# Kernel optimization log

Measured on AMD Instinct MI355X. Metric: run time of the kernel, lower is better.

Reference implementation:

```python
import jax, jax.numpy as jnp
import numpy as np

U, I, D = 100000, 150000, 64
N = U + I
E = 1250000
KEEP_RATE = 0.8


def setup_inputs() -> dict:
    key = jax.random.key(0)
    k1, k2, k3, k4, k5, k6 = jax.random.split(key, 6)
    row = jax.random.randint(k1, (E,), 0, N, dtype=jnp.int32)
    col = jax.random.randint(k2, (E,), 0, N, dtype=jnp.int32)
    adj_values = jax.random.uniform(k3, (E,), dtype=jnp.float32)
    # edge dropout mask: floor(rand + keep_rate) in {0,1}, exactly as SpAdjEdgeDrop
    edge_mask = jnp.floor(jax.random.uniform(k4, (E,), dtype=jnp.float32) + KEEP_RATE)
    user_embeds = jax.random.normal(k5, (U, D), dtype=jnp.float32)
    item_embeds = jax.random.normal(k6, (I, D), dtype=jnp.float32)
    return {
        "row": row,
        "col": col,
        "adj_values": adj_values,
        "edge_mask": edge_mask,
        "user_embeds": user_embeds,
        "item_embeds": item_embeds,
        "layer_num": 3,
    }


def reference(row, col, adj_values, edge_mask, user_embeds, item_embeds, layer_num):
    user_num = user_embeds.shape[0]
    n_nodes = user_num + item_embeds.shape[0]
    # edge-dropped sparse values (mask==0 edges contribute nothing to spmm)
    vals = adj_values * edge_mask  # [E]
    embeds = jnp.concatenate([user_embeds, item_embeds], axis=0)  # [N, D]
    acc = embeds
    cur = embeds
    for _ in range(layer_num):
        # spmm: out[r] += vals[e] * cur[c] for each edge e=(r,c)
        msgs = vals[:, None] * cur[col]  # [E, D] gather
        cur = jax.ops.segment_sum(msgs, row, num_segments=n_nodes)  # [N, D] scatter-add
        acc = acc + cur
    out = acc / (layer_num + 1)
    return out[:user_num], out[user_num:]
```

## Files before the change

kernel.cpp:

```cpp
#include <hip/hip_runtime.h>


#define U_NODES 100000
#define N_NODES 250000
#define DIM4 16
#define E_EDGES 1250000
#define TILE_ROWS 1024
#define NT 245
#define CAP 6144
#define P1_BLOCKS 512

typedef unsigned short u16;

__device__ __forceinline__ float bf2f(u16 h) {
    return __uint_as_float(((unsigned)h) << 16);
}
__device__ __forceinline__ u16 f2bf(float f) {
    unsigned u = __float_as_uint(f);
    u += 0x7fffu + ((u >> 16) & 1u);
    return (u16)(u >> 16);
}
__device__ __forceinline__ ushort4 gat(const u16* __restrict__ base, int node, int part) {
    return ((const ushort4*)(base + ((size_t)node << 6)))[part];
}
__device__ __forceinline__ void fma4(float4& s, float v, ushort4 h) {
    s.x += v * bf2f(h.x);
    s.y += v * bf2f(h.y);
    s.z += v * bf2f(h.z);
    s.w += v * bf2f(h.w);
}

__global__ void lgcn_part(const float4* __restrict__ user4,
                          const float4* __restrict__ item4,
                          u16* __restrict__ e0b,
                          const int* __restrict__ row,
                          const int* __restrict__ col,
                          const float* __restrict__ adj,
                          const float* __restrict__ mask,
                          int* __restrict__ cursors,
                          int2* __restrict__ staging) {
    __shared__ int lhist[NT];
    __shared__ int lbase[NT];
    const int t = threadIdx.x;
    const int gsz = gridDim.x * blockDim.x;
    const int g0 = blockIdx.x * blockDim.x + t;

    for (int i = t; i < NT; i += 256) lhist[i] = 0;
    __syncthreads();

    for (int e = g0; e < E_EDGES; e += gsz)
        if (mask[e] != 0.0f) atomicAdd(&lhist[row[e] >> 10], 1);
    __syncthreads();

    for (int i = t; i < NT; i += 256) {
        int c = lhist[i];
        lbase[i] = c ? atomicAdd(&cursors[i * 16], c) : 0;
        lhist[i] = 0;
    }

    const int CONV = N_NODES * 8;
    for (int i = g0; i < CONV; i += gsz) {
        const int uc = U_NODES * 8;
        const float4* src = (i < uc) ? (user4 + 2 * (long)i)
                                     : (item4 + 2 * (long)(i - uc));
        float4 a = src[0];
        float4 b = src[1];
        int4 o;
        o.x = (int)((unsigned)f2bf(a.x) | ((unsigned)f2bf(a.y) << 16));
        o.y = (int)((unsigned)f2bf(a.z) | ((unsigned)f2bf(a.w) << 16));
        o.z = (int)((unsigned)f2bf(b.x) | ((unsigned)f2bf(b.y) << 16));
        o.w = (int)((unsigned)f2bf(b.z) | ((unsigned)f2bf(b.w) << 16));
        ((int4*)e0b)[i] = o;
    }
    __syncthreads();

    for (int e = g0; e < E_EDGES; e += gsz) {
        float m = mask[e];
        if (m == 0.0f) continue;
        int r = row[e];
        int bkt = r >> 10;
        int rank = lbase[bkt] + atomicAdd(&lhist[bkt], 1);
        if (rank < CAP)
            staging[(size_t)bkt * CAP + rank] =
                make_int2(((r & 1023) << 18) | col[e], __float_as_int(adj[e] * m));
    }
}

__global__ void lgcn_build(const int* __restrict__ cursors,
                           const int2* __restrict__ staging,
                           int* __restrict__ total,
                           int2* __restrict__ rowdesc,
                           int2* __restrict__ csr) {
    __shared__ int lcount[TILE_ROWS];
    __shared__ int lstart[TILE_ROWS];
    __shared__ int lcur[TILE_ROWS];
    __shared__ int lscan[256];
    __shared__ int sbase;
    const int b = blockIdx.x;
    const int t = threadIdx.x;
    const int2* sp = staging + (size_t)b * CAP;
    int cnt = cursors[b * 16];
    if (cnt > CAP) cnt = CAP;

    lcount[t] = 0; lcount[t + 256] = 0; lcount[t + 512] = 0; lcount[t + 768] = 0;
    __syncthreads();
    for (int i = t; i < cnt; i += 256)
        atomicAdd(&lcount[((unsigned)sp[i].x) >> 18], 1);
    __syncthreads();

    int c0 = lcount[4 * t + 0], c1 = lcount[4 * t + 1];
    int c2 = lcount[4 * t + 2], c3 = lcount[4 * t + 3];
    int p0 = (c0 + 3) & ~3, p1 = (c1 + 3) & ~3, p2 = (c2 + 3) & ~3, p3 = (c3 + 3) & ~3;
    int s = p0 + p1 + p2 + p3;
    lscan[t] = s;
    __syncthreads();
    for (int off = 1; off < 256; off <<= 1) {
        int v = (t >= off) ? lscan[t - off] : 0;
        __syncthreads();
        if (t >= off) lscan[t] += v;
        __syncthreads();
    }
    if (t == 255) sbase = atomicAdd(total, lscan[255]);
    __syncthreads();
    const int tilesum = lscan[255];
    int pos = sbase + lscan[t] - s;
    int rbase = b * TILE_ROWS + 4 * t;
    if (rbase + 0 < N_NODES) rowdesc[rbase + 0] = make_int2(pos, c0);
    lstart[4 * t + 0] = pos; lcur[4 * t + 0] = 0; pos += p0;
    if (rbase + 1 < N_NODES) rowdesc[rbase + 1] = make_int2(pos, c1);
    lstart[4 * t + 1] = pos; lcur[4 * t + 1] = 0; pos += p1;
    if (rbase + 2 < N_NODES) rowdesc[rbase + 2] = make_int2(pos, c2);
    lstart[4 * t + 2] = pos; lcur[4 * t + 2] = 0; pos += p2;
    if (rbase + 3 < N_NODES) rowdesc[rbase + 3] = make_int2(pos, c3);
    lstart[4 * t + 3] = pos; lcur[4 * t + 3] = 0;
    __syncthreads();

    for (int i = t; i < tilesum; i += 256) csr[sbase + i] = make_int2(0, 0);
    __syncthreads();

    for (int i = t; i < cnt; i += 256) {
        int2 rec = sp[i];
        int rw = ((unsigned)rec.x) >> 18;
        int rank = atomicAdd(&lcur[rw], 1);
        csr[lstart[rw] + rank] = make_int2(rec.x & 0x3FFFF, rec.y);
    }
}

template <bool LAST>
__global__ void lgcn_pull(const int2* __restrict__ rowdesc,
                          const int2* __restrict__ csr,
                          const u16*  __restrict__ curb,
                          const u16*  __restrict__ e0b,
                          const u16*  __restrict__ e1b,
                          u16*        __restrict__ outb,
                          float4*     __restrict__ out) {
    int tid = blockIdx.x * blockDim.x + threadIdx.x;
    int r = tid >> 4;
    int part = tid & 15;
    if (r >= N_NODES) return;
    int2 rd = rowdesc[r];
    int start = rd.x;
    int pend  = start + ((rd.y + 3) & ~3);
    float4 s = make_float4(0.f, 0.f, 0.f, 0.f);
    int e = start;
    for (; e + 8 <= pend; e += 8) {
        int4 ca = *(const int4*)(csr + e);
        int4 cb = *(const int4*)(csr + e + 2);
        int4 cc = *(const int4*)(csr + e + 4);
        int4 cd = *(const int4*)(csr + e + 6);
        ushort4 h0 = gat(curb, ca.x, part);
        ushort4 h1 = gat(curb, ca.z, part);
        ushort4 h2 = gat(curb, cb.x, part);
        ushort4 h3 = gat(curb, cb.z, part);
        ushort4 h4 = gat(curb, cc.x, part);
        ushort4 h5 = gat(curb, cc.z, part);
        ushort4 h6 = gat(curb, cd.x, part);
        ushort4 h7 = gat(curb, cd.z, part);
        fma4(s, __int_as_float(ca.y), h0);
        fma4(s, __int_as_float(ca.w), h1);
        fma4(s, __int_as_float(cb.y), h2);
        fma4(s, __int_as_float(cb.w), h3);
        fma4(s, __int_as_float(cc.y), h4);
        fma4(s, __int_as_float(cc.w), h5);
        fma4(s, __int_as_float(cd.y), h6);
        fma4(s, __int_as_float(cd.w), h7);
    }
    if (e < pend) {
        int4 ca = *(const int4*)(csr + e);
        int4 cb = *(const int4*)(csr + e + 2);
        ushort4 h0 = gat(curb, ca.x, part);
        ushort4 h1 = gat(curb, ca.z, part);
        ushort4 h2 = gat(curb, cb.x, part);
        ushort4 h3 = gat(curb, cb.z, part);
        fma4(s, __int_as_float(ca.y), h0);
        fma4(s, __int_as_float(ca.w), h1);
        fma4(s, __int_as_float(cb.y), h2);
        fma4(s, __int_as_float(cb.w), h3);
    }
    size_t oi = (size_t)r * DIM4 + part;
    if (LAST) {
        ushort4 a0 = ((const ushort4*)e0b)[oi];
        ushort4 a1 = ((const ushort4*)e1b)[oi];
        ushort4 a2 = ((const ushort4*)curb)[oi];
        out[oi] = make_float4(
            (s.x + bf2f(a0.x) + bf2f(a1.x) + bf2f(a2.x)) * 0.25f,
            (s.y + bf2f(a0.y) + bf2f(a1.y) + bf2f(a2.y)) * 0.25f,
            (s.z + bf2f(a0.z) + bf2f(a1.z) + bf2f(a2.z)) * 0.25f,
            (s.w + bf2f(a0.w) + bf2f(a1.w) + bf2f(a2.w)) * 0.25f);
    } else {
        ((ushort4*)outb)[oi] = make_ushort4(f2bf(s.x), f2bf(s.y), f2bf(s.z), f2bf(s.w));
    }
}

extern "C" void kernel_launch(void* const* d_in, const int* in_sizes, int n_in,
                              void* d_out, int out_size, void* d_ws, size_t ws_size,
                              hipStream_t stream) {
    const int*   row  = (const int*)d_in[0];
    const int*   col  = (const int*)d_in[1];
    const float* adj  = (const float*)d_in[2];
    const float* mask = (const float*)d_in[3];
    const float4* user4 = (const float4*)d_in[4];
    const float4* item4 = (const float4*)d_in[5];

    float4* acc = (float4*)d_out;

    const size_t bemb_bytes = (size_t)N_NODES * 64 * sizeof(u16);
    char* p = (char*)d_ws;
    u16* e0b = (u16*)p;  p += bemb_bytes;
    u16* e1b = (u16*)p;  p += bemb_bytes;
    u16* e2b = (u16*)p;  p += bemb_bytes;
    int* total   = (int*)p;
    int* cursors = (int*)(p + 64);
    p += 64 + (size_t)NT * 64;
    int2* staging = (int2*)p;  p += (size_t)NT * CAP * 8;
    int2* rowdesc = (int2*)p;  p += ((size_t)N_NODES * 8 + 63) & ~63ul;
    int2* csr     = (int2*)p;

    const int BLK = 256;
    const long node_vec4 = (long)N_NODES * DIM4;
    const int  grid_pull = (int)((node_vec4 + BLK - 1) / BLK);

    hipMemsetAsync(total, 0, 64 + (size_t)NT * 64, stream);
    lgcn_part<<<P1_BLOCKS, BLK, 0, stream>>>(user4, item4, e0b, row, col, adj, mask,
                                             cursors, staging);
    lgcn_build<<<NT, BLK, 0, stream>>>(cursors, staging, total, rowdesc, csr);

    lgcn_pull<false><<<grid_pull, BLK, 0, stream>>>(rowdesc, csr, e0b, nullptr, nullptr, e1b, nullptr);
    lgcn_pull<false><<<grid_pull, BLK, 0, stream>>>(rowdesc, csr, e1b, nullptr, nullptr, e2b, nullptr);
    lgcn_pull<true ><<<grid_pull, BLK, 0, stream>>>(rowdesc, csr, e2b, e0b, e1b, nullptr, acc);
}
```

Measured before the change: 296.9 us.

## Replace global bucket cursors with per-block staging segments and offset table

The partition kernel now writes each block's kept edges into its own fixed-size staging segment, ordered by bucket using a local prefix scan. It records per-block bucket offsets in a table, replacing global atomic cursors and the capped shared buckets. The build kernel rebuilds each bucket's edge list by scanning those per-block counts and binary-searching the source segment for every element. This removes global atomics and the CAP overflow limit. In exchange it adds two binary searches per edge and scattered reads across 1024 segments.

```diff
diff --git a/kernel.cpp b/kernel.cpp
--- a/kernel.cpp
+++ b/kernel.cpp
@@ -7,8 +7,9 @@
 #define E_EDGES 1250000
 #define TILE_ROWS 1024
 #define NT 245
-#define CAP 6144
-#define P1_BLOCKS 512
+#define NB 1024
+#define GSZ (NB * 256)
+#define BSEG 1280
 
 typedef unsigned short u16;
 
@@ -37,109 +38,147 @@
                           const int* __restrict__ col,
                           const float* __restrict__ adj,
                           const float* __restrict__ mask,
-                          int* __restrict__ cursors,
+                          int* __restrict__ OFF,
                           int2* __restrict__ staging) {
-    __shared__ int lhist[NT];
-    __shared__ int lbase[NT];
+    __shared__ int lhist[256];
+    __shared__ int lscan[256];
+    __shared__ int loff[256];
+    __shared__ int lcur[256];
     const int t = threadIdx.x;
-    const int gsz = gridDim.x * blockDim.x;
-    const int g0 = blockIdx.x * blockDim.x + t;
-
-    for (int i = t; i < NT; i += 256) lhist[i] = 0;
-    __syncthreads();
-
-    for (int e = g0; e < E_EDGES; e += gsz)
+    const int b = blockIdx.x;
+    const int g0 = b * 256 + t;
+
+    lhist[t] = 0;
+    __syncthreads();
+
+    for (int e = g0; e < E_EDGES; e += GSZ)
         if (mask[e] != 0.0f) atomicAdd(&lhist[row[e] >> 10], 1);
     __syncthreads();
 
-    for (int i = t; i < NT; i += 256) {
-        int c = lhist[i];
-        lbase[i] = c ? atomicAdd(&cursors[i * 16], c) : 0;
-        lhist[i] = 0;
+    int v = lhist[t];
+    lscan[t] = v;
+    __syncthreads();
+    for (int off = 1; off < 256; off <<= 1) {
+        int u = (t >= off) ? lscan[t - off] : 0;
+        __syncthreads();
+        if (t >= off) lscan[t] += u;
+        __syncthreads();
+    }
+    loff[t] = lscan[t] - v;
+    lcur[t] = 0;
+    __syncthreads();
+
+    OFF[b * 256 + t] = loff[t];
+
+    for (int e = g0; e < E_EDGES; e += GSZ) {
+        float m = mask[e];
+        if (m == 0.0f) continue;
+        int r = row[e];
+        int bkt = r >> 10;
+        int rank = loff[bkt] + atomicAdd(&lcur[bkt], 1);
+        staging[(size_t)b * BSEG + rank] =
+            make_int2(((r & 1023) << 18) | col[e], __float_as_int(adj[e] * m));
     }
 
     const int CONV = N_NODES * 8;
-    for (int i = g0; i < CONV; i += gsz) {
+    for (int i = g0; i < CONV; i += GSZ) {
         const int uc = U_NODES * 8;
         const float4* src = (i < uc) ? (user4 + 2 * (long)i)
                                      : (item4 + 2 * (long)(i - uc));
         float4 a = src[0];
-        float4 b = src[1];
+        float4 bb = src[1];
         int4 o;
         o.x = (int)((unsigned)f2bf(a.x) | ((unsigned)f2bf(a.y) << 16));
         o.y = (int)((unsigned)f2bf(a.z) | ((unsigned)f2bf(a.w) << 16));
-        o.z = (int)((unsigned)f2bf(b.x) | ((unsigned)f2bf(b.y) << 16));
-        o.w = (int)((unsigned)f2bf(b.z) | ((unsigned)f2bf(b.w) << 16));
+        o.z = (int)((unsigned)f2bf(bb.x) | ((unsigned)f2bf(bb.y) << 16));
+        o.w = (int)((unsigned)f2bf(bb.z) | ((unsigned)f2bf(bb.w) << 16));
         ((int4*)e0b)[i] = o;
     }
-    __syncthreads();
-
-    for (int e = g0; e < E_EDGES; e += gsz) {
-        float m = mask[e];
-        if (m == 0.0f) continue;
-        int r = row[e];
-        int bkt = r >> 10;
-        int rank = lbase[bkt] + atomicAdd(&lhist[bkt], 1);
-        if (rank < CAP)
-            staging[(size_t)bkt * CAP + rank] =
-                make_int2(((r & 1023) << 18) | col[e], __float_as_int(adj[e] * m));
-    }
-}
-
-__global__ void lgcn_build(const int* __restrict__ cursors,
+}
+
+__global__ void lgcn_build(const int* __restrict__ OFF,
                            const int2* __restrict__ staging,
                            int* __restrict__ total,
                            int2* __restrict__ rowdesc,
                            int2* __restrict__ csr) {
+    __shared__ int S[NB];
+    __shared__ int boff[NB];
     __shared__ int lcount[TILE_ROWS];
     __shared__ int lstart[TILE_ROWS];
     __shared__ int lcur[TILE_ROWS];
     __shared__ int lscan[256];
     __shared__ int sbase;
-    const int b = blockIdx.x;
+    const int i = blockIdx.x;
     const int t = threadIdx.x;
-    const int2* sp = staging + (size_t)b * CAP;
-    int cnt = cursors[b * 16];
-    if (cnt > CAP) cnt = CAP;
-
+
+    int o0 = OFF[(4 * t + 0) * 256 + i], e0 = OFF[(4 * t + 0) * 256 + i + 1];
+    int o1 = OFF[(4 * t + 1) * 256 + i], e1 = OFF[(4 * t + 1) * 256 + i + 1];
+    int o2 = OFF[(4 * t + 2) * 256 + i], e2 = OFF[(4 * t + 2) * 256 + i + 1];
+    int o3 = OFF[(4 * t + 3) * 256 + i], e3 = OFF[(4 * t + 3) * 256 + i + 1];
+    int c0 = e0 - o0, c1 = e1 - o1, c2 = e2 - o2, c3 = e3 - o3;
+    boff[4 * t + 0] = o0; boff[4 * t + 1] = o1;
+    boff[4 * t + 2] = o2; boff[4 * t + 3] = o3;
+    int sl = c0 + c1 + c2 + c3;
+    lscan[t] = sl;
+    __syncthreads();
+    for (int off = 1; off < 256; off <<= 1) {
+        int u = (t >= off) ? lscan[t - off] : 0;
+        __syncthreads();
+        if (t >= off) lscan[t] += u;
+        __syncthreads();
+    }
+    int ex = lscan[t] - sl;
+    S[4 * t + 0] = ex;
+    S[4 * t + 1] = ex + c0;
+    S[4 * t + 2] = ex + c0 + c1;
+    S[4 * t + 3] = ex + c0 + c1 + c2;
+    const int T = lscan[255];
     lcount[t] = 0; lcount[t + 256] = 0; lcount[t + 512] = 0; lcount[t + 768] = 0;
     __syncthreads();
-    for (int i = t; i < cnt; i += 256)
-        atomicAdd(&lcount[((unsigned)sp[i].x) >> 18], 1);
-    __syncthreads();
-
-    int c0 = lcount[4 * t + 0], c1 = lcount[4 * t + 1];
-    int c2 = lcount[4 * t + 2], c3 = lcount[4 * t + 3];
-    int p0 = (c0 + 3) & ~3, p1 = (c1 + 3) & ~3, p2 = (c2 + 3) & ~3, p3 = (c3 + 3) & ~3;
+
+    for (int j = t; j < T; j += 256) {
+        int lo = 0, hi = NB;
+        while (hi - lo > 1) { int mid = (lo + hi) >> 1; if (S[mid] <= j) lo = mid; else hi = mid; }
+        int2 rec = staging[(size_t)lo * BSEG + boff[lo] + (j - S[lo])];
+        atomicAdd(&lcount[((unsigned)rec.x) >> 18], 1);
+    }
+    __syncthreads();
+
+    int d0 = lcount[4 * t + 0], d1 = lcount[4 * t + 1];
+    int d2 = lcount[4 * t + 2], d3 = lcount[4 * t + 3];
+    int p0 = (d0 + 3) & ~3, p1 = (d1 + 3) & ~3, p2 = (d2 + 3) & ~3, p3 = (d3 + 3) & ~3;
     int s = p0 + p1 + p2 + p3;
+    __syncthreads();
     lscan[t] = s;
     __syncthreads();
     for (int off = 1; off < 256; off <<= 1) {
-        int v = (t >= off) ? lscan[t - off] : 0;
-        __syncthreads();
-        if (t >= off) lscan[t] += v;
+        int u = (t >= off) ? lscan[t - off] : 0;
+        __syncthreads();
+        if (t >= off) lscan[t] += u;
         __syncthreads();
     }
     if (t == 255) sbase = atomicAdd(total, lscan[255]);
     __syncthreads();
     const int tilesum = lscan[255];
     int pos = sbase + lscan[t] - s;
-    int rbase = b * TILE_ROWS + 4 * t;
-    if (rbase + 0 < N_NODES) rowdesc[rbase + 0] = make_int2(pos, c0);
+    int rbase = i * TILE_ROWS + 4 * t;
+    if (rbase + 0 < N_NODES) rowdesc[rbase + 0] = make_int2(pos, d0);
     lstart[4 * t + 0] = pos; lcur[4 * t + 0] = 0; pos += p0;
-    if (rbase + 1 < N_NODES) rowdesc[rbase + 1] = make_int2(pos, c1);
+    if (rbase + 1 < N_NODES) rowdesc[rbase + 1] = make_int2(pos, d1);
     lstart[4 * t + 1] = pos; lcur[4 * t + 1] = 0; pos += p1;
-    if (rbase + 2 < N_NODES) rowdesc[rbase + 2] = make_int2(pos, c2);
+    if (rbase + 2 < N_NODES) rowdesc[rbase + 2] = make_int2(pos, d2);
     lstart[4 * t + 2] = pos; lcur[4 * t + 2] = 0; pos += p2;
-    if (rbase + 3 < N_NODES) rowdesc[rbase + 3] = make_int2(pos, c3);
+    if (rbase + 3 < N_NODES) rowdesc[rbase + 3] = make_int2(pos, d3);
     lstart[4 * t + 3] = pos; lcur[4 * t + 3] = 0;
     __syncthreads();
 
-    for (int i = t; i < tilesum; i += 256) csr[sbase + i] = make_int2(0, 0);
-    __syncthreads();
-
-    for (int i = t; i < cnt; i += 256) {
-        int2 rec = sp[i];
+    for (int j = t; j < tilesum; j += 256) csr[sbase + j] = make_int2(0, 0);
+    __syncthreads();
+
+    for (int j = t; j < T; j += 256) {
+        int lo = 0, hi = NB;
+        while (hi - lo > 1) { int mid = (lo + hi) >> 1; if (S[mid] <= j) lo = mid; else hi = mid; }
+        int2 rec = staging[(size_t)lo * BSEG + boff[lo] + (j - S[lo])];
         int rw = ((unsigned)rec.x) >> 18;
         int rank = atomicAdd(&lcur[rw], 1);
         csr[lstart[rw] + rank] = make_int2(rec.x & 0x3FFFF, rec.y);
@@ -229,10 +268,9 @@
     u16* e0b = (u16*)p;  p += bemb_bytes;
     u16* e1b = (u16*)p;  p += bemb_bytes;
     u16* e2b = (u16*)p;  p += bemb_bytes;
-    int* total   = (int*)p;
-    int* cursors = (int*)(p + 64);
-    p += 64 + (size_t)NT * 64;
-    int2* staging = (int2*)p;  p += (size_t)NT * CAP * 8;
+    int* total = (int*)p;  p += 64;
+    int* OFF   = (int*)p;  p += (size_t)NB * 256 * 4;
+    int2* staging = (int2*)p;  p += (size_t)NB * BSEG * 8;
     int2* rowdesc = (int2*)p;  p += ((size_t)N_NODES * 8 + 63) & ~63ul;
     int2* csr     = (int2*)p;
 
@@ -240,10 +278,10 @@
     const long node_vec4 = (long)N_NODES * DIM4;
     const int  grid_pull = (int)((node_vec4 + BLK - 1) / BLK);
 
-    hipMemsetAsync(total, 0, 64 + (size_t)NT * 64, stream);
-    lgcn_part<<<P1_BLOCKS, BLK, 0, stream>>>(user4, item4, e0b, row, col, adj, mask,
-                                             cursors, staging);
-    lgcn_build<<<NT, BLK, 0, stream>>>(cursors, staging, total, rowdesc, csr);
+    hipMemsetAsync(total, 0, 64, stream);
+    lgcn_part<<<NB, BLK, 0, stream>>>(user4, item4, e0b, row, col, adj, mask,
+                                      OFF, staging);
+    lgcn_build<<<NT, BLK, 0, stream>>>(OFF, staging, total, rowdesc, csr);
 
     lgcn_pull<false><<<grid_pull, BLK, 0, stream>>>(rowdesc, csr, e0b, nullptr, nullptr, e1b, nullptr);
     lgcn_pull<false><<<grid_pull, BLK, 0, stream>>>(rowdesc, csr, e1b, nullptr, nullptr, e2b, nullptr);
```

New measurement: 304.0 us. +2.4%, slower.
